# Kernel optimization log

Measured on AMD Instinct MI355X. Metric: run time of the kernel, lower is better.

Reference implementation:

```python
import jax, jax.numpy as jnp
import numpy as np

N = 4096
IN_DIM = 1433
HID = 64
OUT_DIM = 7
LAM_HAT = 0.9
LAM = 1.0 / LAM_HAT - 1.0          # skip-connection weight lambda
SCAD_A = 3.7
K_STEPS = 10
AVG_DEG = 32


def setup_inputs() -> dict:
    key = jax.random.key(0)
    k_a, k_x, k_w1, k_w2 = jax.random.split(key, 4)
    # symmetric binary adjacency, avg degree ~AVG_DEG, zero diagonal
    U = jax.random.uniform(k_a, (N, N), dtype=jnp.float32)
    p = AVG_DEG / N
    A = (jnp.minimum(U, U.T) < p).astype(jnp.float32)
    A = A * (1.0 - jnp.eye(N, dtype=jnp.float32))
    X = jax.random.normal(k_x, (N, IN_DIM), dtype=jnp.float32)
    w1 = jax.random.normal(k_w1, (IN_DIM, HID), dtype=jnp.float32) * (1.0 / np.sqrt(IN_DIM))
    b1 = jnp.zeros((HID,), dtype=jnp.float32)
    w2 = jax.random.normal(k_w2, (HID, OUT_DIM), dtype=jnp.float32) * (1.0 / np.sqrt(HID))
    b2 = jnp.zeros((OUT_DIM,), dtype=jnp.float32)
    log_gamma_0 = jnp.asarray(np.log(3.0), dtype=jnp.float32)          # gamma_0_init = 3.0
    raw_decay = jnp.asarray(np.log(0.85 / 0.15), dtype=jnp.float32)    # logit(0.85)
    return {"A": A, "X": X, "w1": w1, "b1": b1, "w2": w2, "b2": b2,
            "log_gamma_0": log_gamma_0, "raw_decay": raw_decay}


def _scad_weight(y, lam_k):
    """SCAD IRLS edge weight: 1 for y<=lam, linear roll-off to 0 at y=a*lam."""
    y_safe = jnp.maximum(y, 1e-12)  # avoid 0/0 in unselected branch
    w_mid = (SCAD_A * lam_k - y) / ((SCAD_A - 1.0) * y_safe)
    return jnp.where(y <= lam_k, 1.0,
                     jnp.where(y <= SCAD_A * lam_k, w_mid, 0.0))


def reference(A, X, w1, b1, w2, b2, log_gamma_0, raw_decay):
    # 1. MLP (eval mode: dropout = identity): X -> F0 in class space [N, C]
    F0 = jax.nn.relu(X @ w1 + b1) @ w2 + b2

    n = A.shape[0]
    eye = jnp.eye(n, dtype=A.dtype)
    A = A + eye                                   # add_loops
    D = A.sum(-1)                                 # [N]
    D_sq = jnp.sqrt(D)[:, None]                   # [N,1]
    d_is = 1.0 / jnp.sqrt(D)
    A_tilde = A * d_is[:, None] * d_is[None, :]   # sym_norm

    g0 = jnp.exp(log_gamma_0)
    r = jax.nn.sigmoid(raw_decay)

    F = F0
    for k in range(K_STEPS):
        gamma_k = g0 * (r ** k)
        lam_k = gamma_k / SCAD_A
        # pairwise squared Euclidean of degree-normalized features (detached)
        Fn = jax.lax.stop_gradient(F / D_sq)      # [N,C]
        sq = jnp.sum(Fn * Fn, axis=-1)
        Z = jnp.maximum(sq[:, None] + sq[None, :] - 2.0 * (Fn @ Fn.T), 0.0)
        y = jnp.sqrt(Z)                           # [N,N]
        W = _scad_weight(y, lam_k)
        W = W * (1.0 - eye)                       # zero diagonal
        W = jnp.where(jnp.isnan(W), 1.0, W)       # NaN guard (as in torch code)
        Q_hat = ((W * A).sum(-1) / D + LAM)[:, None]   # [N,1]
        F = (W * A_tilde) @ F / Q_hat + LAM * F0 / Q_hat
    return F


if __name__ == "__main__":
    out = reference(**setup_inputs())
    print(out.shape, out.dtype)
```

## Files before the change

kernel.cpp:

```cpp
#include <hip/hip_runtime.h>
#include <math.h>

#define N_NODES 4096
#define IN_DIM  1433
#define HID     64
#define OUT_DIM 7
#define FPAD    8
#define CAP     128
#define BR      64
#define KT      32
#define LPN     16

static constexpr float LAMBDA = (float)(1.0 / 0.9 - 1.0);
static constexpr float SCADA  = 3.7f;

__global__ __launch_bounds__(256) void front(const float* __restrict__ A,
    const float* __restrict__ X, const float* __restrict__ w1,
    int* __restrict__ nbr, int* __restrict__ cnt, float* __restrict__ deg,
    float* __restrict__ rsd, float* __restrict__ P, float* __restrict__ lamt,
    const float* __restrict__ lg0p, const float* __restrict__ rdp, int ksplit) {
  __shared__ __align__(16) float lds[KT * (BR + 4) + KT * HID];
  const int b = blockIdx.x;
  const int t = threadIdx.x;

  if (b < N_NODES) {
    const int i = b;
    if (i == 0 && t == 0) {
      float r_ = 1.0f / (1.0f + expf(-rdp[0]));
      float g  = expf(lg0p[0]) * (1.0f / SCADA);
      #pragma unroll
      for (int k = 0; k < 10; ++k) { lamt[k] = g; g *= r_; }
    }
    int* cp = (int*)lds;
    if (t == 0) *cp = 0;
    __syncthreads();
    const float4* row = (const float4*)(A + (size_t)i * N_NODES);
    for (int q = t; q < N_NODES / 4; q += 256) {
      float4 v = row[q];
      int j0 = q * 4;
      if (v.x != 0.0f) { int s = atomicAdd(cp, 1); if (s < CAP) nbr[(size_t)i * CAP + s] = j0; }
      if (v.y != 0.0f) { int s = atomicAdd(cp, 1); if (s < CAP) nbr[(size_t)i * CAP + s] = j0 + 1; }
      if (v.z != 0.0f) { int s = atomicAdd(cp, 1); if (s < CAP) nbr[(size_t)i * CAP + s] = j0 + 2; }
      if (v.w != 0.0f) { int s = atomicAdd(cp, 1); if (s < CAP) nbr[(size_t)i * CAP + s] = j0 + 3; }
    }
    __syncthreads();
    if (t == 0) {
      int cc = *cp; if (cc > CAP) cc = CAP;
      cnt[i] = cc;
      float d = (float)(*cp) + 1.0f;
      deg[i] = d;
      rsd[i] = 1.0f / sqrtf(d);
    }
    return;
  }

  const int bb = b - N_NODES;
  const int rb = bb & (N_NODES / BR - 1);
  const int ks = bb >> 6;
  const int r0 = rb * BR;
  const int kbeg = (IN_DIM * ks) / ksplit;
  const int kend = (IN_DIM * (ks + 1)) / ksplit;
  const int rg = t >> 4;
  const int cg = t & 15;
  float* Xs = lds;
  float* Ws = lds + KT * (BR + 4);

  float acc[4][4];
  #pragma unroll
  for (int r = 0; r < 4; ++r)
    #pragma unroll
    for (int c = 0; c < 4; ++c) acc[r][c] = 0.0f;

  for (int k0 = kbeg; k0 < kend; k0 += KT) {
    #pragma unroll
    for (int j = 0; j < (BR * KT) / 256; ++j) {
      int e = t + 256 * j;
      int row = e >> 5;
      int kk  = e & (KT - 1);
      int k   = k0 + kk;
      float v = (k < kend) ? X[(size_t)(r0 + row) * IN_DIM + k] : 0.0f;
      Xs[kk * (BR + 4) + row] = v;
    }
    #pragma unroll
    for (int j = 0; j < (HID * KT) / 256; ++j) {
      int e = t + 256 * j;
      int kk  = e >> 6;
      int col = e & 63;
      int k   = k0 + kk;
      Ws[kk * HID + col] = (k < kend) ? w1[(size_t)k * HID + col] : 0.0f;
    }
    __syncthreads();
    #pragma unroll
    for (int kk = 0; kk < KT; ++kk) {
      const float4 xv = *(const float4*)&Xs[kk * (BR + 4) + rg * 4];
      const float4 wv = *(const float4*)&Ws[kk * HID + cg * 4];
      float xr[4] = {xv.x, xv.y, xv.z, xv.w};
      float wc[4] = {wv.x, wv.y, wv.z, wv.w};
      #pragma unroll
      for (int r = 0; r < 4; ++r)
        #pragma unroll
        for (int c = 0; c < 4; ++c) acc[r][c] += xr[r] * wc[c];
    }
    __syncthreads();
  }
  float* Pp = P + (size_t)ks * N_NODES * HID;
  #pragma unroll
  for (int r = 0; r < 4; ++r) {
    int row = r0 + rg * 4 + r;
    float4 v = make_float4(acc[r][0], acc[r][1], acc[r][2], acc[r][3]);
    *(float4*)&Pp[(size_t)row * HID + cg * 4] = v;
  }
}

__global__ __launch_bounds__(256) void reduce_mlp(const float* __restrict__ P,
    const float* __restrict__ b1, const float* __restrict__ w2,
    const float* __restrict__ b2, float* __restrict__ F0,
    float* __restrict__ Fcur, int ksplit) {
  const int wave = threadIdx.x >> 6;
  const int lane = threadIdx.x & 63;
  const int row  = blockIdx.x * 4 + wave;

  float h = 0.0f;
  const float* p = P + (size_t)row * HID + lane;
  for (int ks = 0; ks < ksplit; ++ks)
    h += p[(size_t)ks * N_NODES * HID];
  float hv = fmaxf(h + b1[lane], 0.0f);

  float a0 = hv * w2[lane * OUT_DIM + 0];
  float a1 = hv * w2[lane * OUT_DIM + 1];
  float a2 = hv * w2[lane * OUT_DIM + 2];
  float a3 = hv * w2[lane * OUT_DIM + 3];
  float a4 = hv * w2[lane * OUT_DIM + 4];
  float a5 = hv * w2[lane * OUT_DIM + 5];
  float a6 = hv * w2[lane * OUT_DIM + 6];
  #pragma unroll
  for (int off = 32; off > 0; off >>= 1) {
    a0 += __shfl_xor(a0, off);
    a1 += __shfl_xor(a1, off);
    a2 += __shfl_xor(a2, off);
    a3 += __shfl_xor(a3, off);
    a4 += __shfl_xor(a4, off);
    a5 += __shfl_xor(a5, off);
    a6 += __shfl_xor(a6, off);
  }
  if (lane == 0) {
    float o[FPAD] = {a0 + b2[0], a1 + b2[1], a2 + b2[2], a3 + b2[3],
                     a4 + b2[4], a5 + b2[5], a6 + b2[6], 0.0f};
    float4 v0 = make_float4(o[0], o[1], o[2], o[3]);
    float4 v1 = make_float4(o[4], o[5], o[6], o[7]);
    float4* f0p = (float4*)(F0  + (size_t)row * FPAD);
    float4* fcp = (float4*)(Fcur + (size_t)row * FPAD);
    f0p[0] = v0; f0p[1] = v1;
    fcp[0] = v0; fcp[1] = v1;
  }
}

__global__ __launch_bounds__(256) void rung_step(const float* __restrict__ Fin,
    const float* __restrict__ F0, float* __restrict__ Fout,
    const int* __restrict__ nbr, const int* __restrict__ cnt,
    const float* __restrict__ deg, const float* __restrict__ rsd,
    const float* __restrict__ lamt, int kstep, int last) {
  const int lane = threadIdx.x & (LPN - 1);
  const int i = (blockIdx.x * 256 + threadIdx.x) / LPN;

  const float lam = lamt[kstep];
  const float rsi = rsd[i];
  const float Di  = deg[i];
  const int   ci  = cnt[i];

  float Fni[FPAD];
  {
    const float4* fp = (const float4*)(Fin + (size_t)i * FPAD);
    float4 a0 = fp[0], a1 = fp[1];
    Fni[0] = a0.x * rsi; Fni[1] = a0.y * rsi; Fni[2] = a0.z * rsi; Fni[3] = a0.w * rsi;
    Fni[4] = a1.x * rsi; Fni[5] = a1.y * rsi; Fni[6] = a1.z * rsi; Fni[7] = a1.w * rsi;
  }
  float s = 0.0f;
  float acc[FPAD] = {0, 0, 0, 0, 0, 0, 0, 0};
  const int* nb = nbr + (size_t)i * CAP;
  for (int l = lane; l < ci; l += LPN) {
    int j = nb[l];
    float rsj = rsd[j];
    const float4* fp = (const float4*)(Fin + (size_t)j * FPAD);
    float4 b0 = fp[0], b1v = fp[1];
    float fj[FPAD] = {b0.x, b0.y, b0.z, b0.w, b1v.x, b1v.y, b1v.z, b1v.w};
    float d2 = 0.0f;
    #pragma unroll
    for (int c = 0; c < FPAD; ++c) {
      float df = Fni[c] - fj[c] * rsj;
      d2 += df * df;
    }
    float y = sqrtf(d2);
    float w;
    if (y <= lam)              w = 1.0f;
    else if (y <= SCADA * lam) w = (SCADA * lam - y) / ((SCADA - 1.0f) * fmaxf(y, 1e-12f));
    else                       w = 0.0f;
    if (w != w) w = 1.0f;
    s += w;
    float wr = w * rsi * rsj;
    #pragma unroll
    for (int c = 0; c < FPAD; ++c) acc[c] += wr * fj[c];
  }
  #pragma unroll
  for (int off = LPN / 2; off > 0; off >>= 1) {
    s += __shfl_xor(s, off, LPN);
    #pragma unroll
    for (int c = 0; c < FPAD; ++c) acc[c] += __shfl_xor(acc[c], off, LPN);
  }
  if (lane == 0) {
    float Q = s / Di + LAMBDA;
    float inv = 1.0f / Q;
    if (last) {
      #pragma unroll
      for (int c = 0; c < OUT_DIM; ++c)
        Fout[(size_t)i * OUT_DIM + c] = (acc[c] + LAMBDA * F0[(size_t)i * FPAD + c]) * inv;
    } else {
      float o[FPAD];
      #pragma unroll
      for (int c = 0; c < FPAD; ++c)
        o[c] = (acc[c] + LAMBDA * F0[(size_t)i * FPAD + c]) * inv;
      float4* op = (float4*)(Fout + (size_t)i * FPAD);
      op[0] = make_float4(o[0], o[1], o[2], o[3]);
      op[1] = make_float4(o[4], o[5], o[6], o[7]);
    }
  }
}

extern "C" void kernel_launch(void* const* d_in, const int* in_sizes, int n_in,
                              void* d_out, int out_size, void* d_ws, size_t ws_size,
                              hipStream_t stream) {
  const float* A   = (const float*)d_in[0];
  const float* X   = (const float*)d_in[1];
  const float* w1  = (const float*)d_in[2];
  const float* b1  = (const float*)d_in[3];
  const float* w2  = (const float*)d_in[4];
  const float* b2  = (const float*)d_in[5];
  const float* lg0 = (const float*)d_in[6];
  const float* rd  = (const float*)d_in[7];
  float* out = (float*)d_out;

  const size_t fixed = (size_t)N_NODES * CAP * sizeof(int)
                     + (size_t)N_NODES * sizeof(int)
                     + (size_t)N_NODES * sizeof(float) * 2
                     + (size_t)N_NODES * FPAD * sizeof(float) * 3
                     + 64;
  const size_t pbuf = (size_t)N_NODES * HID * sizeof(float);
  int ksplit = (ws_size >= fixed + 16 * pbuf) ? 16 : 8;

  char* w = (char*)d_ws;
  int*   nbr = (int*)w;   w += (size_t)N_NODES * CAP * sizeof(int);
  int*   cnt = (int*)w;   w += (size_t)N_NODES * sizeof(int);
  float* deg = (float*)w; w += (size_t)N_NODES * sizeof(float);
  float* rsd = (float*)w; w += (size_t)N_NODES * sizeof(float);
  float* P   = (float*)w; w += (size_t)ksplit * N_NODES * HID * sizeof(float);
  float* F0  = (float*)w; w += (size_t)N_NODES * FPAD * sizeof(float);
  float* FA  = (float*)w; w += (size_t)N_NODES * FPAD * sizeof(float);
  float* FB  = (float*)w; w += (size_t)N_NODES * FPAD * sizeof(float);
  float* lamt = (float*)w;

  front<<<N_NODES + (N_NODES / BR) * ksplit, 256, 0, stream>>>(
      A, X, w1, nbr, cnt, deg, rsd, P, lamt, lg0, rd, ksplit);
  reduce_mlp<<<N_NODES / 4, 256, 0, stream>>>(P, b1, w2, b2, F0, FA, ksplit);

  float* cur = FA;
  float* nxt = FB;
  for (int k = 0; k < 10; ++k) {
    int last = (k == 9);
    float* dst = last ? out : nxt;
    rung_step<<<(N_NODES * LPN) / 256, 256, 0, stream>>>(cur, F0, dst, nbr, cnt,
                                                         deg, rsd, lamt, k, last);
    float* tmp = cur; cur = nxt; nxt = tmp;
  }
}
```

Measured before the change: 206.7 us.

## Split fused front kernel into adjacency build and split-K GEMM kernels

The single heterogeneous front kernel, which mixed adjacency-row scanning blocks with X@w1 GEMM blocks, is split into two launches: build_adj and gemm1 on a 2D grid. The GEMM can now use its own LDS allocation, and w1 tiles are loaded as float4. The split-K factor can rise to 32 when the workspace is large enough, giving more GEMM blocks. The cost is an extra kernel launch, the loss of concurrency between the two workloads, and more partial buffers for reduce_mlp to sum.

```diff
diff --git a/kernel.cpp b/kernel.cpp
--- a/kernel.cpp
+++ b/kernel.cpp
@@ -14,56 +14,50 @@
 static constexpr float LAMBDA = (float)(1.0 / 0.9 - 1.0);
 static constexpr float SCADA  = 3.7f;
 
-__global__ __launch_bounds__(256) void front(const float* __restrict__ A,
-    const float* __restrict__ X, const float* __restrict__ w1,
+__global__ __launch_bounds__(256) void build_adj(const float* __restrict__ A,
     int* __restrict__ nbr, int* __restrict__ cnt, float* __restrict__ deg,
-    float* __restrict__ rsd, float* __restrict__ P, float* __restrict__ lamt,
-    const float* __restrict__ lg0p, const float* __restrict__ rdp, int ksplit) {
-  __shared__ __align__(16) float lds[KT * (BR + 4) + KT * HID];
-  const int b = blockIdx.x;
-  const int t = threadIdx.x;
-
-  if (b < N_NODES) {
-    const int i = b;
-    if (i == 0 && t == 0) {
-      float r_ = 1.0f / (1.0f + expf(-rdp[0]));
-      float g  = expf(lg0p[0]) * (1.0f / SCADA);
-      #pragma unroll
-      for (int k = 0; k < 10; ++k) { lamt[k] = g; g *= r_; }
-    }
-    int* cp = (int*)lds;
-    if (t == 0) *cp = 0;
-    __syncthreads();
-    const float4* row = (const float4*)(A + (size_t)i * N_NODES);
-    for (int q = t; q < N_NODES / 4; q += 256) {
-      float4 v = row[q];
-      int j0 = q * 4;
-      if (v.x != 0.0f) { int s = atomicAdd(cp, 1); if (s < CAP) nbr[(size_t)i * CAP + s] = j0; }
-      if (v.y != 0.0f) { int s = atomicAdd(cp, 1); if (s < CAP) nbr[(size_t)i * CAP + s] = j0 + 1; }
-      if (v.z != 0.0f) { int s = atomicAdd(cp, 1); if (s < CAP) nbr[(size_t)i * CAP + s] = j0 + 2; }
-      if (v.w != 0.0f) { int s = atomicAdd(cp, 1); if (s < CAP) nbr[(size_t)i * CAP + s] = j0 + 3; }
-    }
-    __syncthreads();
-    if (t == 0) {
-      int cc = *cp; if (cc > CAP) cc = CAP;
-      cnt[i] = cc;
-      float d = (float)(*cp) + 1.0f;
-      deg[i] = d;
-      rsd[i] = 1.0f / sqrtf(d);
-    }
-    return;
-  }
-
-  const int bb = b - N_NODES;
-  const int rb = bb & (N_NODES / BR - 1);
-  const int ks = bb >> 6;
-  const int r0 = rb * BR;
+    float* __restrict__ rsd, float* __restrict__ lamt,
+    const float* __restrict__ lg0p, const float* __restrict__ rdp) {
+  int i = blockIdx.x;
+  if (i == 0 && threadIdx.x == 0) {
+    float r_ = 1.0f / (1.0f + expf(-rdp[0]));
+    float g  = expf(lg0p[0]) * (1.0f / SCADA);
+    #pragma unroll
+    for (int k = 0; k < 10; ++k) { lamt[k] = g; g *= r_; }
+  }
+  __shared__ int c;
+  if (threadIdx.x == 0) c = 0;
+  __syncthreads();
+  const float4* row = (const float4*)(A + (size_t)i * N_NODES);
+  for (int q = threadIdx.x; q < N_NODES / 4; q += 256) {
+    float4 v = row[q];
+    int j0 = q * 4;
+    if (v.x != 0.0f) { int s = atomicAdd(&c, 1); if (s < CAP) nbr[(size_t)i * CAP + s] = j0; }
+    if (v.y != 0.0f) { int s = atomicAdd(&c, 1); if (s < CAP) nbr[(size_t)i * CAP + s] = j0 + 1; }
+    if (v.z != 0.0f) { int s = atomicAdd(&c, 1); if (s < CAP) nbr[(size_t)i * CAP + s] = j0 + 2; }
+    if (v.w != 0.0f) { int s = atomicAdd(&c, 1); if (s < CAP) nbr[(size_t)i * CAP + s] = j0 + 3; }
+  }
+  __syncthreads();
+  if (threadIdx.x == 0) {
+    int cc = c; if (cc > CAP) cc = CAP;
+    cnt[i] = cc;
+    float d = (float)c + 1.0f;
+    deg[i] = d;
+    rsd[i] = 1.0f / sqrtf(d);
+  }
+}
+
+__global__ __launch_bounds__(256) void gemm1(const float* __restrict__ X,
+    const float* __restrict__ w1, float* __restrict__ P, int ksplit) {
+  __shared__ __align__(16) float Xs[KT][BR + 4];
+  __shared__ __align__(16) float Ws[KT][HID];
+  const int t  = threadIdx.x;
+  const int r0 = blockIdx.x * BR;
+  const int ks = blockIdx.y;
   const int kbeg = (IN_DIM * ks) / ksplit;
   const int kend = (IN_DIM * (ks + 1)) / ksplit;
   const int rg = t >> 4;
   const int cg = t & 15;
-  float* Xs = lds;
-  float* Ws = lds + KT * (BR + 4);
 
   float acc[4][4];
   #pragma unroll
@@ -79,21 +73,23 @@
       int kk  = e & (KT - 1);
       int k   = k0 + kk;
       float v = (k < kend) ? X[(size_t)(r0 + row) * IN_DIM + k] : 0.0f;
-      Xs[kk * (BR + 4) + row] = v;
-    }
-    #pragma unroll
-    for (int j = 0; j < (HID * KT) / 256; ++j) {
-      int e = t + 256 * j;
-      int kk  = e >> 6;
-      int col = e & 63;
-      int k   = k0 + kk;
-      Ws[kk * HID + col] = (k < kend) ? w1[(size_t)k * HID + col] : 0.0f;
+      Xs[kk][row] = v;
+    }
+    #pragma unroll
+    for (int j = 0; j < (HID * KT) / (256 * 4); ++j) {
+      int f = t + 256 * j;
+      int kk   = f >> 4;
+      int colq = f & 15;
+      int k    = k0 + kk;
+      float4 v = make_float4(0.f, 0.f, 0.f, 0.f);
+      if (k < kend) v = *(const float4*)&w1[(size_t)k * HID + colq * 4];
+      *(float4*)&Ws[kk][colq * 4] = v;
     }
     __syncthreads();
     #pragma unroll
     for (int kk = 0; kk < KT; ++kk) {
-      const float4 xv = *(const float4*)&Xs[kk * (BR + 4) + rg * 4];
-      const float4 wv = *(const float4*)&Ws[kk * HID + cg * 4];
+      const float4 xv = *(const float4*)&Xs[kk][rg * 4];
+      const float4 wv = *(const float4*)&Ws[kk][cg * 4];
       float xr[4] = {xv.x, xv.y, xv.z, xv.w};
       float wc[4] = {wv.x, wv.y, wv.z, wv.w};
       #pragma unroll
@@ -245,7 +241,8 @@
                      + (size_t)N_NODES * FPAD * sizeof(float) * 3
                      + 64;
   const size_t pbuf = (size_t)N_NODES * HID * sizeof(float);
-  int ksplit = (ws_size >= fixed + 16 * pbuf) ? 16 : 8;
+  int ksplit = (ws_size >= fixed + 32 * pbuf) ? 32
+             : (ws_size >= fixed + 16 * pbuf) ? 16 : 8;
 
   char* w = (char*)d_ws;
   int*   nbr = (int*)w;   w += (size_t)N_NODES * CAP * sizeof(int);
@@ -258,8 +255,8 @@
   float* FB  = (float*)w; w += (size_t)N_NODES * FPAD * sizeof(float);
   float* lamt = (float*)w;
 
-  front<<<N_NODES + (N_NODES / BR) * ksplit, 256, 0, stream>>>(
-      A, X, w1, nbr, cnt, deg, rsd, P, lamt, lg0, rd, ksplit);
+  build_adj<<<N_NODES, 256, 0, stream>>>(A, nbr, cnt, deg, rsd, lamt, lg0, rd);
+  gemm1<<<dim3(N_NODES / BR, ksplit), 256, 0, stream>>>(X, w1, P, ksplit);
   reduce_mlp<<<N_NODES / 4, 256, 0, stream>>>(P, b1, w2, b2, F0, FA, ksplit);
 
   float* cur = FA;
```

Result: slower. 212.9 us (+3.0%).
